# Performance work log

Measured on AMD Instinct MI355X. Metric: run time of the kernel, lower is better.

The kernel has to match this reference:

```python
import jax, jax.numpy as jnp
import numpy as np
from jax import lax

M, T, WINDOW = 4096, 2048, 25
NEG_DIAG = -1e10  # matches alphas.fill_diagonal_(-1e10)


def setup_inputs() -> dict:
    key = jax.random.key(0)
    k_ys, k_a, k_r, k_b0, k_b1 = jax.random.split(key, 5)
    ys = jax.random.uniform(k_ys, (M, T), dtype=jnp.float32) * 10.0  # case counts
    alphas = 0.01 * jax.random.normal(k_a, (M, M), dtype=jnp.float32)
    repro = 1.0 + 0.01 * jax.random.normal(k_r, (M, WINDOW), dtype=jnp.float32)  # init ones
    b0 = 0.1 * jax.random.normal(k_b0, (M, 1), dtype=jnp.float32)
    b1 = 0.01 * jax.random.normal(k_b1, (M, 1), dtype=jnp.float32)
    t = jnp.arange(T, dtype=jnp.int32) + 1
    return {"ys": ys, "alphas": alphas, "repro": repro, "b0": b0, "b1": b1, "t": t}


def reference(ys, alphas, repro, b0, b1, t):
    m, _ = ys.shape
    window = repro.shape[1]
    offset = window - 1
    # metapopulation weights: sigmoid adjacency with diagonal forced to ~0
    diag = jnp.eye(m, dtype=bool)
    W = jax.nn.sigmoid(jnp.where(diag, jnp.asarray(NEG_DIAG, ys.dtype), alphas))
    # depthwise conv1d (cross-correlation), groups=M, VALID padding -> (M, T-window+1)
    Z = lax.conv_general_dilated(
        ys[None],                 # (1, M, T)
        repro[:, None, :],        # (M, 1, window)
        window_strides=(1,),
        padding='VALID',
        feature_group_count=m,
        dimension_numbers=('NCH', 'OIH', 'NCH'),
    )[0]                          # (M, T')
    ys_n = ys[:, offset:]         # (M, T')
    # beta_net: per-node softplus-linear in time -> (M, T), then narrow
    tt = t.astype(ys.dtype)
    beta = jax.nn.softplus(b0 + b1 * tt[None, :])[:, offset:]  # (M, T')
    return beta * (jax.nn.softplus(Z) + W @ ys_n)
```

## Files before the change

### kernel.cpp

```cpp
#include <hip/hip_runtime.h>
#include <stdint.h>

#define M_DIM 4096
#define T_DIM 2048
#define N_OUT 2024
#define N_PAD 2048
#define WIN   25
#define K_DIM 4096

typedef float f32x4 __attribute__((ext_vector_type(4)));

__device__ __forceinline__ unsigned short f2bf(float x) {
  unsigned u = __float_as_uint(x);
  u += 0x7FFF + ((u >> 16) & 1);
  return (unsigned short)(u >> 16);
}
__device__ __forceinline__ float bf2f(unsigned short h) {
  return __uint_as_float(((unsigned)h) << 16);
}

__device__ __forceinline__ void gl2lds16(const void* g, void* l) {
  __builtin_amdgcn_global_load_lds(
      (const __attribute__((address_space(1))) unsigned int*)g,
      (__attribute__((address_space(3))) unsigned int*)l, 16, 0, 0);
}

__device__ __forceinline__ int pk_fp8x4(float a, float b, float c, float d) {
  int w = __builtin_amdgcn_cvt_pk_fp8_f32(a, b, 0, false);
  w = __builtin_amdgcn_cvt_pk_fp8_f32(c, d, w, true);
  return w;
}

__global__ __launch_bounds__(256) void k_wcast(const float* __restrict__ alphas,
                                               unsigned char* __restrict__ W8) {
  size_t i8 = ((size_t)blockIdx.x * 256 + threadIdx.x) * 8;
  const float4 v0 = *(const float4*)(alphas + i8);
  const float4 v1 = *(const float4*)(alphas + i8 + 4);
  int row = (int)(i8 >> 12);
  int col = (int)(i8 & 4095);
  float a[8] = {v0.x, v0.y, v0.z, v0.w, v1.x, v1.y, v1.z, v1.w};
  float w[8];
#pragma unroll
  for (int j = 0; j < 8; ++j)
    w[j] = (row == col + j) ? 0.f : 1.f / (1.f + __expf(-a[j]));
  int p0 = pk_fp8x4(w[0], w[1], w[2], w[3]);
  int p1 = pk_fp8x4(w[4], w[5], w[6], w[7]);
  *(uint2*)(W8 + i8) = uint2{(unsigned)p0, (unsigned)p1};
}

__global__ __launch_bounds__(256) void k_convT(const float* __restrict__ ys,
                                               const float* __restrict__ repro,
                                               unsigned short* __restrict__ Sbf,
                                               unsigned char* __restrict__ BT8) {
  __shared__ float sy[32][284];
  __shared__ float sr[32][26];
  const int tid = threadIdx.x;
  const int c0 = blockIdx.x * 256;
  const int m0 = blockIdx.y * 32;

  for (int slot = tid; slot < 32 * 70; slot += 256) {
    int r = slot / 70, f = slot % 70;
    int c = c0 + f * 4;
    float4 v = (c < T_DIM) ? *(const float4*)(ys + (size_t)(m0 + r) * T_DIM + c)
                           : float4{0.f, 0.f, 0.f, 0.f};
    sy[r][f * 4 + 0] = v.x; sy[r][f * 4 + 1] = v.y;
    sy[r][f * 4 + 2] = v.z; sy[r][f * 4 + 3] = v.w;
  }
  for (int slot = tid; slot < 32 * WIN; slot += 256) {
    int r = slot / WIN, k = slot % WIN;
    sr[r][k] = repro[(m0 + r) * WIN + k];
  }
  __syncthreads();

  {
    const int r = tid >> 3;
    const int cbase = (tid & 7) * 32;
    float y[56];
#pragma unroll
    for (int i = 0; i < 56; ++i) y[i] = sy[r][cbase + i];
    float rv[WIN];
#pragma unroll
    for (int k = 0; k < WIN; ++k) rv[k] = sr[r][k];
    unsigned pk[16];
#pragma unroll
    for (int jj = 0; jj < 32; ++jj) {
      float z = 0.f;
#pragma unroll
      for (int k = 0; k < WIN; ++k) z += y[jj + k] * rv[k];
      float sp = fmaxf(z, 0.f) + log1pf(__expf(-fabsf(z)));
      int gj = c0 + cbase + jj;
      unsigned short h = (gj < N_OUT) ? f2bf(sp) : (unsigned short)0;
      if (jj & 1) pk[jj >> 1] |= ((unsigned)h) << 16;
      else        pk[jj >> 1]  = (unsigned)h;
    }
    unsigned short* dst = Sbf + (size_t)(m0 + r) * N_PAD + c0 + cbase;
    *(uint4*)(dst)      = *(const uint4*)(pk + 0);
    *(uint4*)(dst + 8)  = *(const uint4*)(pk + 4);
    *(uint4*)(dst + 16) = *(const uint4*)(pk + 8);
    *(uint4*)(dst + 24) = *(const uint4*)(pk + 12);
  }

  {
    const int n = c0 + tid;
    const bool ok = (n < N_OUT);
    unsigned w[8];
#pragma unroll
    for (int i = 0; i < 8; ++i) {
      float a0 = ok ? sy[4 * i + 0][tid + 24] : 0.f;
      float a1 = ok ? sy[4 * i + 1][tid + 24] : 0.f;
      float a2 = ok ? sy[4 * i + 2][tid + 24] : 0.f;
      float a3 = ok ? sy[4 * i + 3][tid + 24] : 0.f;
      w[i] = (unsigned)pk_fp8x4(a0, a1, a2, a3);
    }
    unsigned char* dst = BT8 + (size_t)n * K_DIM + m0;
    *(uint4*)(dst)      = uint4{w[0], w[1], w[2], w[3]};
    *(uint4*)(dst + 16) = uint4{w[4], w[5], w[6], w[7]};
  }
}

__global__ __launch_bounds__(1024, 4) void k_gemm(const unsigned char* __restrict__ W8,
                                                  const unsigned char* __restrict__ BT8,
                                                  const unsigned short* __restrict__ Sbf,
                                                  const float* __restrict__ b0,
                                                  const float* __restrict__ b1,
                                                  float* __restrict__ out) {
  __shared__ __align__(64) unsigned char lA[2][256 * 64];
  __shared__ __align__(64) unsigned char lB[2][128 * 64];
  const int tid  = threadIdx.x;
  const int wave = tid >> 6;
  const int lane = tid & 63;
  const int wm = wave >> 2;
  const int wn = wave & 3;
  const int m16  = lane & 15;
  const int quad = lane >> 4;

  const int fid  = blockIdx.y * gridDim.x + blockIdx.x;
  const int swz  = (fid & 7) * 32 + (fid >> 3);
  const int tileN = (swz & 15) * 128;
  const int tileM = (swz >> 4) * 256;

  const int key  = (m16 >> 1) & 3;
  const int sub  = (quad & 1) * 8;
  const int rowA = (wm * 64 + m16) * 64;
  const int rowB = (wn * 32 + m16) * 64;
  int hOf[2];
#pragma unroll
  for (int h = 0; h < 2; ++h)
    hOf[h] = (((2 * h + (quad >> 1)) ^ key) << 4) + sub;

  const int oA = tid * 16;
  const int rA = oA >> 6;
  const int sA = (oA >> 4) & 3;
  const int qA = sA ^ ((rA >> 1) & 3);
  const unsigned char* gA = W8 + (size_t)(tileM + rA) * K_DIM + qA * 16;
  const int rB = (tid * 16) >> 6;
  const int qB = (((tid * 16) >> 4) & 3) ^ ((rB >> 1) & 3);
  const unsigned char* gB = BT8 + (size_t)(tileN + rB) * K_DIM + qB * 16;
  const int ldsBase = wave * 1024;

  f32x4 acc[4][2];
#pragma unroll
  for (int i = 0; i < 4; ++i)
#pragma unroll
    for (int j = 0; j < 2; ++j) acc[i][j] = f32x4{0.f, 0.f, 0.f, 0.f};

  auto stage = [&](int buf, int kt_) {
    const size_t kb_ = (size_t)kt_ * 64;
    gl2lds16(gA + kb_, &lA[buf][ldsBase]);
    if (wave < 8) gl2lds16(gB + kb_, &lB[buf][ldsBase]);
  };
  auto compute = [&](int buf) {
#pragma unroll
    for (int h = 0; h < 2; ++h) {
      long long aF[4], bF[2];
#pragma unroll
      for (int i = 0; i < 4; ++i)
        aF[i] = *(const long long*)&lA[buf][rowA + i * 1024 + hOf[h]];
#pragma unroll
      for (int j = 0; j < 2; ++j)
        bF[j] = *(const long long*)&lB[buf][rowB + j * 1024 + hOf[h]];
#pragma unroll
      for (int i = 0; i < 4; ++i)
#pragma unroll
        for (int j = 0; j < 2; ++j)
          acc[i][j] = __builtin_amdgcn_mfma_f32_16x16x32_fp8_fp8(
              aF[i], bF[j], acc[i][j], 0, 0, 0);
    }
  };

  stage(0, 0);

#pragma unroll 1
  for (int kt = 0; kt < K_DIM / 64; kt += 2) {
    stage(1, kt + 1);
    if (wave < 8) {
      asm volatile("s_waitcnt vmcnt(2)" ::: "memory");
    } else {
      asm volatile("s_waitcnt vmcnt(1)" ::: "memory");
    }
    __builtin_amdgcn_s_barrier();
    asm volatile("" ::: "memory");
    compute(0);
    __builtin_amdgcn_s_barrier();
    asm volatile("" ::: "memory");

    if (kt + 2 < K_DIM / 64) {
      stage(0, kt + 2);
      if (wave < 8) {
        asm volatile("s_waitcnt vmcnt(2)" ::: "memory");
      } else {
        asm volatile("s_waitcnt vmcnt(1)" ::: "memory");
      }
    } else {
      asm volatile("s_waitcnt vmcnt(0)" ::: "memory");
    }
    __builtin_amdgcn_s_barrier();
    asm volatile("" ::: "memory");
    compute(1);
    __builtin_amdgcn_s_barrier();
    asm volatile("" ::: "memory");
  }

#pragma unroll
  for (int j = 0; j < 2; ++j) {
    int gn = tileN + wn * 32 + j * 16 + m16;
    if (gn >= N_OUT) continue;
    float tval = (float)(gn + WIN);
#pragma unroll
    for (int i = 0; i < 4; ++i) {
#pragma unroll
      for (int r2 = 0; r2 < 4; ++r2) {
        int gm = tileM + wm * 64 + i * 16 + quad * 4 + r2;
        float x = b0[gm] + b1[gm] * tval;
        float beta = fmaxf(x, 0.f) + log1pf(__expf(-fabsf(x)));
        float sv = bf2f(Sbf[(size_t)gm * N_PAD + gn]);
        out[(size_t)gm * N_OUT + gn] = beta * (sv + acc[i][j][r2]);
      }
    }
  }
}

extern "C" void kernel_launch(void* const* d_in, const int* in_sizes, int n_in,
                              void* d_out, int out_size, void* d_ws, size_t ws_size,
                              hipStream_t stream) {
  const float* ys     = (const float*)d_in[0];
  const float* alphas = (const float*)d_in[1];
  const float* repro  = (const float*)d_in[2];
  const float* b0     = (const float*)d_in[3];
  const float* b1     = (const float*)d_in[4];
  float* out = (float*)d_out;

  char* ws = (char*)d_ws;
  unsigned char*  W8  = (unsigned char*)ws;
  unsigned char*  BT8 = (unsigned char*)(ws + (size_t)M_DIM * K_DIM);
  unsigned short* Sbf = (unsigned short*)(ws + (size_t)M_DIM * K_DIM
                                             + (size_t)N_PAD * K_DIM);

  k_wcast<<<(M_DIM * (size_t)K_DIM) / 8 / 256, 256, 0, stream>>>(alphas, W8);
  k_convT<<<dim3(T_DIM / 256, M_DIM / 32), 256, 0, stream>>>(ys, repro, Sbf, BT8);
  k_gemm<<<dim3(N_PAD / 128, M_DIM / 256), 1024, 0, stream>>>(W8, BT8, Sbf,
                                                              b0, b1, out);
}
```

Baseline: 263.0 us.

## Retile FP8 GEMM to 128x128 blocks with 128-deep K steps and 512 threads

Changes the GEMM block tile from 256x128 with K-step 64 and 1024 threads to 128x128 with K-step 128 and 512 threads. Each wave now issues two A and two B global-to-LDS loads per stage, and the LDS swizzle widens to 8 chunks. The goal is to halve the number of K-loop barriers and give every wave balanced loads, at the cost of more blocks and less A-operand reuse per block.

```diff
diff --git a/kernel.cpp b/kernel.cpp
--- a/kernel.cpp
+++ b/kernel.cpp
@@ -118,14 +118,14 @@
   }
 }
 
-__global__ __launch_bounds__(1024, 4) void k_gemm(const unsigned char* __restrict__ W8,
-                                                  const unsigned char* __restrict__ BT8,
-                                                  const unsigned short* __restrict__ Sbf,
-                                                  const float* __restrict__ b0,
-                                                  const float* __restrict__ b1,
-                                                  float* __restrict__ out) {
-  __shared__ __align__(64) unsigned char lA[2][256 * 64];
-  __shared__ __align__(64) unsigned char lB[2][128 * 64];
+__global__ __launch_bounds__(512, 4) void k_gemm(const unsigned char* __restrict__ W8,
+                                                 const unsigned char* __restrict__ BT8,
+                                                 const unsigned short* __restrict__ Sbf,
+                                                 const float* __restrict__ b0,
+                                                 const float* __restrict__ b1,
+                                                 float* __restrict__ out) {
+  __shared__ __align__(64) unsigned char lA[2][128 * 128];
+  __shared__ __align__(64) unsigned char lB[2][128 * 128];
   const int tid  = threadIdx.x;
   const int wave = tid >> 6;
   const int lane = tid & 63;
@@ -135,28 +135,32 @@
   const int quad = lane >> 4;
 
   const int fid  = blockIdx.y * gridDim.x + blockIdx.x;
-  const int swz  = (fid & 7) * 32 + (fid >> 3);
+  const int swz  = (fid & 7) * 64 + (fid >> 3);
   const int tileN = (swz & 15) * 128;
-  const int tileM = (swz >> 4) * 256;
-
-  const int key  = (m16 >> 1) & 3;
+  const int tileM = (swz >> 4) * 128;
+
+  const int key  = (m16 >> 1) & 7;
   const int sub  = (quad & 1) * 8;
-  const int rowA = (wm * 64 + m16) * 64;
-  const int rowB = (wn * 32 + m16) * 64;
-  int hOf[2];
-#pragma unroll
-  for (int h = 0; h < 2; ++h)
+  const int rowA = (wm * 64 + m16) * 128;
+  const int rowB = (wn * 32 + m16) * 128;
+  int hOf[4];
+#pragma unroll
+  for (int h = 0; h < 4; ++h)
     hOf[h] = (((2 * h + (quad >> 1)) ^ key) << 4) + sub;
 
-  const int oA = tid * 16;
-  const int rA = oA >> 6;
-  const int sA = (oA >> 4) & 3;
-  const int qA = sA ^ ((rA >> 1) & 3);
-  const unsigned char* gA = W8 + (size_t)(tileM + rA) * K_DIM + qA * 16;
-  const int rB = (tid * 16) >> 6;
-  const int qB = (((tid * 16) >> 4) & 3) ^ ((rB >> 1) & 3);
-  const unsigned char* gB = BT8 + (size_t)(tileN + rB) * K_DIM + qB * 16;
-  const int ldsBase = wave * 1024;
+  const unsigned char* gA[2];
+  const unsigned char* gB[2];
+  int ldsBase[2];
+#pragma unroll
+  for (int c = 0; c < 2; ++c) {
+    int o = c * 8192 + wave * 1024 + lane * 16;
+    int r = o >> 7;
+    int s = (o >> 4) & 7;
+    int q = s ^ ((r >> 1) & 7);
+    gA[c] = W8  + (size_t)(tileM + r) * K_DIM + q * 16;
+    gB[c] = BT8 + (size_t)(tileN + r) * K_DIM + q * 16;
+    ldsBase[c] = c * 8192 + wave * 1024;
+  }
 
   f32x4 acc[4][2];
 #pragma unroll
@@ -165,20 +169,23 @@
     for (int j = 0; j < 2; ++j) acc[i][j] = f32x4{0.f, 0.f, 0.f, 0.f};
 
   auto stage = [&](int buf, int kt_) {
-    const size_t kb_ = (size_t)kt_ * 64;
-    gl2lds16(gA + kb_, &lA[buf][ldsBase]);
-    if (wave < 8) gl2lds16(gB + kb_, &lB[buf][ldsBase]);
+    const size_t kb_ = (size_t)kt_ * 128;
+#pragma unroll
+    for (int c = 0; c < 2; ++c) {
+      gl2lds16(gA[c] + kb_, &lA[buf][ldsBase[c]]);
+      gl2lds16(gB[c] + kb_, &lB[buf][ldsBase[c]]);
+    }
   };
   auto compute = [&](int buf) {
 #pragma unroll
-    for (int h = 0; h < 2; ++h) {
+    for (int h = 0; h < 4; ++h) {
       long long aF[4], bF[2];
 #pragma unroll
       for (int i = 0; i < 4; ++i)
-        aF[i] = *(const long long*)&lA[buf][rowA + i * 1024 + hOf[h]];
+        aF[i] = *(const long long*)&lA[buf][rowA + i * 2048 + hOf[h]];
 #pragma unroll
       for (int j = 0; j < 2; ++j)
-        bF[j] = *(const long long*)&lB[buf][rowB + j * 1024 + hOf[h]];
+        bF[j] = *(const long long*)&lB[buf][rowB + j * 2048 + hOf[h]];
 #pragma unroll
       for (int i = 0; i < 4; ++i)
 #pragma unroll
@@ -191,26 +198,18 @@
   stage(0, 0);
 
 #pragma unroll 1
-  for (int kt = 0; kt < K_DIM / 64; kt += 2) {
+  for (int kt = 0; kt < K_DIM / 128; kt += 2) {
     stage(1, kt + 1);
-    if (wave < 8) {
-      asm volatile("s_waitcnt vmcnt(2)" ::: "memory");
-    } else {
-      asm volatile("s_waitcnt vmcnt(1)" ::: "memory");
-    }
+    asm volatile("s_waitcnt vmcnt(4)" ::: "memory");
     __builtin_amdgcn_s_barrier();
     asm volatile("" ::: "memory");
     compute(0);
     __builtin_amdgcn_s_barrier();
     asm volatile("" ::: "memory");
 
-    if (kt + 2 < K_DIM / 64) {
+    if (kt + 2 < K_DIM / 128) {
       stage(0, kt + 2);
-      if (wave < 8) {
-        asm volatile("s_waitcnt vmcnt(2)" ::: "memory");
-      } else {
-        asm volatile("s_waitcnt vmcnt(1)" ::: "memory");
-      }
+      asm volatile("s_waitcnt vmcnt(4)" ::: "memory");
     } else {
       asm volatile("s_waitcnt vmcnt(0)" ::: "memory");
     }
@@ -258,6 +257,6 @@
 
   k_wcast<<<(M_DIM * (size_t)K_DIM) / 8 / 256, 256, 0, stream>>>(alphas, W8);
   k_convT<<<dim3(T_DIM / 256, M_DIM / 32), 256, 0, stream>>>(ys, repro, Sbf, BT8);
-  k_gemm<<<dim3(N_PAD / 128, M_DIM / 256), 1024, 0, stream>>>(W8, BT8, Sbf,
-                                                              b0, b1, out);
-}
+  k_gemm<<<dim3(N_PAD / 128, M_DIM / 128), 512, 0, stream>>>(W8, BT8, Sbf,
+                                                             b0, b1, out);
+}
```

Result: faster. 248.9 us (-5.4%).
